# Performance work log

Measured on AMD Instinct MI355X. Metric: run time of the kernel, lower is better.

Reference implementation:

```python
import jax, jax.numpy as jnp
import numpy as np

THRESH = 0.4


def setup_inputs() -> dict:
    key = jax.random.key(0)
    ks = jax.random.split(key, 8)
    B, N, C, H, O = 8, 16384, 640, 256, 128
    s = 0.02  # small init so sigmoid(logits) ~ 0.5 -> realistic mixed selection
    return {
        "point_features": jax.random.normal(ks[0], (B, N, C), jnp.float32),
        "point_coords": jax.random.normal(ks[1], (B, N, 3), jnp.float32) * 10.0,
        "w1": jax.random.normal(ks[2], (C, H), jnp.float32) * s,
        "b1": jnp.zeros((H,), jnp.float32),
        "w2": jax.random.normal(ks[3], (H, 1), jnp.float32) * s,
        "b2": jnp.zeros((1,), jnp.float32),
        "wo": jax.random.normal(ks[4], (C, O), jnp.float32) * s,
        "bo": jnp.zeros((O,), jnp.float32),
    }


def reference(point_features, point_coords, w1, b1, w2, b2, wo, bo):
    B, N, _ = point_features.shape
    # 2-layer MLP -> per-point logit -> sigmoid score
    h = jax.nn.relu(jnp.einsum('bnc,ch->bnh', point_features, w1) + b1)
    logits = jnp.einsum('bnh,ho->bno', h, w2) + b2          # [B, N, 1]
    scores = jax.nn.sigmoid(logits)                          # [B, N, 1]
    # score-scaled features through output projection
    feats = jnp.einsum('bnc,co->bno', point_features * scores, wo) + bo  # [B, N, O]
    # score-threshold selection + per-batch stream compaction into a
    # zero-padded tensor (padded to N, the jit-static worst case)
    sel = scores[..., 0] > THRESH                            # [B, N] bool
    pos = jnp.cumsum(sel.astype(jnp.int32), axis=1) - 1      # destination slot
    pos = jnp.where(sel, pos, N)                             # unselected -> OOB (dropped)
    bidx = jnp.arange(B)[:, None]
    selected_keypoints = jnp.zeros_like(feats).at[bidx, pos].set(feats, mode='drop')
    selected_coords = jnp.zeros_like(point_coords).at[bidx, pos].set(point_coords, mode='drop')
    # point_mask: True where the row is zero padding (matches (coords==0).sum(-1)!=0)
    point_mask = jnp.sum(selected_coords == 0, axis=-1) != 0
    return selected_keypoints, selected_coords, point_mask
```

## Files before the change

kernel.cpp:

```cpp
#include <hip/hip_runtime.h>
#include <hip/hip_bf16.h>


typedef __attribute__((ext_vector_type(8))) short short8v;
typedef __attribute__((ext_vector_type(4))) float f32x4;

#define M_TOTAL 131072
#define C_DIM 640
#define H_DIM 256
#define O_DIM 128
#define NCOMB 384
#define TM 64
#define KSTEPS 20
#define N_PTS 16384
#define TILES_PER_B 256
#define NTILES 2048
#define THRL -0.4054651081f
#define FIX_MARGIN 0.03f

#define OUT_COORD_OFF 16777216
#define OUT_MASK_OFF  17170432

#define WT_OFF     0u
#define TMASK_OFF  491520u
#define TAGG_OFF   507904u
#define TEXCL_OFF  516096u
#define COUNTS_OFF 524288u
#define G_OFF      1572864u

#define LGKMCNT0 asm volatile("s_waitcnt lgkmcnt(0)" ::: "memory")
#define SBAR __builtin_amdgcn_s_barrier()

__device__ __forceinline__ unsigned int f2bf_bits(float f) {
  unsigned int u = __builtin_bit_cast(unsigned int, f);
  return (u + 0x7fffu + ((u >> 16) & 1u)) >> 16;
}
__device__ __forceinline__ unsigned int pack_bf2(float lo, float hi) {
  return f2bf_bits(lo) | (f2bf_bits(hi) << 16);
}

__global__ __launch_bounds__(256) void convert_w(const float* __restrict__ w1,
                                                 const float* __restrict__ wo,
                                                 unsigned short* __restrict__ Wt2) {
  int o = blockIdx.x * 256 + threadIdx.x;
  if (o < NCOMB * C_DIM) {
    int e = o & 7;
    int g = o >> 3;
    int pp = g & 3;
    int qq = (g >> 2) & 15;
    int tc = g >> 6;
    int ct = tc % 24;
    int t = tc / 24;
    int k = t * 32 + pp * 8 + e;
    int n = ct * 16 + qq;
    float v = (n < H_DIM) ? w1[k * H_DIM + n] : wo[k * O_DIM + (n - H_DIM)];
    Wt2[o] = (unsigned short)f2bf_bits(v);
  }
}

__global__ __launch_bounds__(512, 4) void gemm_fused(
    const float* __restrict__ pf, const unsigned short* __restrict__ Wt2,
    const float* __restrict__ w1, const float* __restrict__ b1,
    const float* __restrict__ w2, const float* __restrict__ b2,
    const float* __restrict__ bo, unsigned long long* __restrict__ tmask,
    int* __restrict__ tagg, float* __restrict__ G) {
  __shared__ __align__(16) unsigned short As[3][2048];

  const int tid = threadIdx.x;
  const int lane = tid & 63;
  const int wv = tid >> 6;
  const int q = lane & 15;
  const int p = lane >> 4;
  const int tile = blockIdx.x;
  const int m0 = tile * TM;

  f32x4 acc[3][4];
#pragma unroll
  for (int i = 0; i < 3; ++i)
#pragma unroll
    for (int rt = 0; rt < 4; ++rt) acc[i][rt] = (f32x4){0.f, 0.f, 0.f, 0.f};

  const float* asrc = pf + (size_t)(m0 + (tid >> 3)) * C_DIM + (tid & 7) * 4;
  const int aphys = ((tid >> 1) ^ ((tid >> 4) & 3)) * 8 + (tid & 1) * 4;
  const int aswz = (q >> 1) & 3;

  const unsigned short* bbase = Wt2 + wv * 512 + q * 32 + p * 8;

  float4 Rcur;
  {
    float4 R0 = *(const float4*)(asrc);
    Rcur = *(const float4*)(asrc + 32);
    *(uint2*)&As[0][aphys] = make_uint2(pack_bf2(R0.x, R0.y), pack_bf2(R0.z, R0.w));
    LGKMCNT0;
    SBAR;
  }

  int scur = 0;
#pragma unroll 1
  for (int t = 0; t < KSTEPS; ++t) {
    const unsigned short* bp = bbase + (size_t)t * 12288;
    short8v bc0 = *(const short8v*)(bp);
    short8v bc1 = *(const short8v*)(bp + 4096);
    short8v bc2 = *(const short8v*)(bp + 8192);
    int snxt = scur + 1;
    if (snxt == 3) snxt = 0;
    if (t + 2 < KSTEPS) {
      float4 Rnext = *(const float4*)(asrc + (t + 2) * 32);
      *(uint2*)&As[snxt][aphys] =
          make_uint2(pack_bf2(Rcur.x, Rcur.y), pack_bf2(Rcur.z, Rcur.w));
      Rcur = Rnext;
    } else if (t + 1 < KSTEPS) {
      *(uint2*)&As[snxt][aphys] =
          make_uint2(pack_bf2(Rcur.x, Rcur.y), pack_bf2(Rcur.z, Rcur.w));
    }
    LGKMCNT0;
    SBAR;
    short8v af[4];
#pragma unroll
    for (int rt = 0; rt < 4; ++rt)
      af[rt] = *(const short8v*)&As[scur][((rt * 64 + q * 4 + p) ^ aswz) * 8];
    __builtin_amdgcn_s_setprio(1);
#pragma unroll
    for (int rt = 0; rt < 4; ++rt) {
      acc[0][rt] = __builtin_amdgcn_mfma_f32_16x16x32_bf16(af[rt], bc0, acc[0][rt], 0, 0, 0);
      acc[1][rt] = __builtin_amdgcn_mfma_f32_16x16x32_bf16(af[rt], bc1, acc[1][rt], 0, 0, 0);
      acc[2][rt] = __builtin_amdgcn_mfma_f32_16x16x32_bf16(af[rt], bc2, acc[2][rt], 0, 0, 0);
    }
    __builtin_amdgcn_s_setprio(0);
    scur = snxt;
  }
  __syncthreads();

  float* lpart = (float*)&As[0][0];
  float* llog = (float*)&As[1][0];
  float* srow = llog + 64;
  float* fsum = srow + 64;
  unsigned long long* s_fixmask = (unsigned long long*)(fsum + 4);

  float w2v[2], b1v[2];
#pragma unroll
  for (int i = 0; i < 2; ++i) {
    int col = (wv + 8 * i) * 16 + q;
    w2v[i] = w2[col];
    b1v[i] = b1[col];
  }
#pragma unroll
  for (int rt = 0; rt < 4; ++rt) {
    float pr[4] = {0.f, 0.f, 0.f, 0.f};
#pragma unroll
    for (int i = 0; i < 2; ++i)
#pragma unroll
      for (int r = 0; r < 4; ++r)
        pr[r] += fmaxf(acc[i][rt][r] + b1v[i], 0.f) * w2v[i];
#pragma unroll
    for (int mk = 1; mk < 16; mk <<= 1)
#pragma unroll
      for (int r = 0; r < 4; ++r) pr[r] += __shfl_xor(pr[r], mk);
    if (q == 0)
#pragma unroll
      for (int r = 0; r < 4; ++r) lpart[wv * 64 + rt * 16 + p * 4 + r] = pr[r];
  }
  __syncthreads();

  bool nf = false;
  if (wv == 0) {
    float lg = b2[0];
#pragma unroll
    for (int w = 0; w < 8; ++w) lg += lpart[w * 64 + tid];
    llog[tid] = lg;
    nf = fabsf(lg - THRL) < FIX_MARGIN;
  }
  unsigned long long fm = __ballot(nf);
  if (tid == 0) *s_fixmask = fm;
  __syncthreads();

  unsigned long long fixmask = *s_fixmask;
  while (fixmask) {
    int row = __ffsll(fixmask) - 1;
    fixmask &= fixmask - 1;
    if (tid < 256) {
      const float* prow = pf + (size_t)(m0 + row) * C_DIM;
      float a0 = 0.f, a1 = 0.f;
      for (int c = 0; c < C_DIM; c += 2) {
        a0 = fmaf(prow[c], w1[(size_t)c * H_DIM + tid], a0);
        a1 = fmaf(prow[c + 1], w1[(size_t)(c + 1) * H_DIM + tid], a1);
      }
      float v = fmaxf(a0 + a1 + b1[tid], 0.f) * w2[tid];
#pragma unroll
      for (int mk = 1; mk < 64; mk <<= 1) v += __shfl_xor(v, mk);
      if (lane == 0) fsum[wv] = v;
    }
    __syncthreads();
    if (tid == 0)
      llog[row] = fsum[0] + fsum[1] + fsum[2] + fsum[3] + b2[0];
    __syncthreads();
  }

  bool sel = false;
  float flog = 0.f;
  if (wv == 0) {
    flog = llog[tid];
    sel = flog > THRL;
  }
  unsigned long long selmask = __ballot(sel);
  if (wv == 0) {
    srow[tid] = 1.f / (1.f + expf(-flog));
    if (tid == 0) {
      tmask[tile] = selmask;
      tagg[tile] = __popcll(selmask);
    }
  }
  __syncthreads();

  {
    const int gcol = wv * 16 + q;
    const float bov = bo[gcol];
#pragma unroll
    for (int rt = 0; rt < 4; ++rt)
#pragma unroll
      for (int r = 0; r < 4; ++r) {
        int row = rt * 16 + p * 4 + r;
        G[(size_t)(m0 + row) * O_DIM + gcol] = fmaf(acc[2][rt][r], srow[row], bov);
      }
  }
}

__global__ __launch_bounds__(256) void scan_tiles(const int* __restrict__ tagg,
                                                  int* __restrict__ texcl,
                                                  int* __restrict__ counts) {
  __shared__ int wsum[4];
  const int c = blockIdx.x, t = threadIdx.x;
  const int lane = t & 63, w = t >> 6;
  int v = tagg[c * 256 + t];
  int inc = v;
#pragma unroll
  for (int d = 1; d < 64; d <<= 1) {
    int n = __shfl_up(inc, d);
    if (lane >= d) inc += n;
  }
  if (lane == 63) wsum[w] = inc;
  __syncthreads();
  int base = 0;
#pragma unroll
  for (int ww = 0; ww < 4; ++ww)
    if (ww < w) base += wsum[ww];
  texcl[c * 256 + t] = base + inc - v;
  if (t == 255) counts[c] = base + inc;
}

__global__ __launch_bounds__(512) void scatter(
    const float* __restrict__ G, const unsigned long long* __restrict__ tmask,
    const int* __restrict__ texcl, const float* __restrict__ pc,
    float* __restrict__ out) {
  const int tile = blockIdx.x;
  const int tid = threadIdx.x;
  const int lane = tid & 63;
  const int wv = tid >> 6;
  const unsigned long long mask = tmask[tile];
  const int base = (tile >> 8) * N_PTS + texcl[tile];
  const int m0 = tile * TM;
#pragma unroll
  for (int j = 0; j < 8; ++j) {
    const int row = wv * 8 + j;
    if (!((mask >> row) & 1ull)) continue;
    const int dst = base + __popcll(mask & ((1ull << row) - 1ull));
    const int m = m0 + row;
    float2 g = *(const float2*)(G + (size_t)m * O_DIM + lane * 2);
    *(float2*)(out + (size_t)dst * O_DIM + lane * 2) = g;
    if (lane == 0) {
      float c0 = pc[m * 3], c1 = pc[m * 3 + 1], c2 = pc[m * 3 + 2];
      float* oc = out + OUT_COORD_OFF;
      oc[dst * 3] = c0; oc[dst * 3 + 1] = c1; oc[dst * 3 + 2] = c2;
      out[OUT_MASK_OFF + dst] = (c0 == 0.f || c1 == 0.f || c2 == 0.f) ? 1.f : 0.f;
    }
  }
}

__global__ __launch_bounds__(256) void fill_tail(const int* __restrict__ counts,
                                                 float* __restrict__ out) {
  const int lane = threadIdx.x & 63;
  for (int m = blockIdx.x * 4 + (threadIdx.x >> 6); m < M_TOTAL; m += 8192) {
    int b = m >> 14, j = m & (N_PTS - 1);
    if (j < counts[b]) continue;
    *(float2*)(out + (size_t)m * O_DIM + lane * 2) = make_float2(0.f, 0.f);
    if (lane == 0) {
      float* oc = out + OUT_COORD_OFF;
      oc[m * 3] = 0.f; oc[m * 3 + 1] = 0.f; oc[m * 3 + 2] = 0.f;
      out[OUT_MASK_OFF + m] = 1.f;
    }
  }
}

extern "C" void kernel_launch(void* const* d_in, const int* in_sizes, int n_in,
                              void* d_out, int out_size, void* d_ws, size_t ws_size,
                              hipStream_t stream) {
  const float* pf = (const float*)d_in[0];
  const float* pc = (const float*)d_in[1];
  const float* w1 = (const float*)d_in[2];
  const float* b1 = (const float*)d_in[3];
  const float* w2 = (const float*)d_in[4];
  const float* b2 = (const float*)d_in[5];
  const float* wo = (const float*)d_in[6];
  const float* bo = (const float*)d_in[7];
  float* out = (float*)d_out;
  char* ws = (char*)d_ws;

  unsigned short* Wt2 = (unsigned short*)(ws + WT_OFF);
  unsigned long long* tmask = (unsigned long long*)(ws + TMASK_OFF);
  int* tagg = (int*)(ws + TAGG_OFF);
  int* texcl = (int*)(ws + TEXCL_OFF);
  int* counts = (int*)(ws + COUNTS_OFF);
  float* G = (float*)(ws + G_OFF);

  convert_w<<<960, 256, 0, stream>>>(w1, wo, Wt2);
  gemm_fused<<<NTILES, 512, 0, stream>>>(pf, Wt2, w1, b1, w2, b2, bo,
                                         tmask, tagg, G);
  scan_tiles<<<8, 256, 0, stream>>>(tagg, texcl, counts);
  scatter<<<NTILES, 512, 0, stream>>>(G, tmask, texcl, pc, out);
  fill_tail<<<2048, 256, 0, stream>>>(counts, out);
}
```

Measured before the change: 197.5 us.

## Replicate bf16 weights, rotate K-step start per tile, prefetch B fragments

The converted weight buffer is written four times, and each tile reads the copy chosen by tile&3. Each tile also starts its K loop at a tile-dependent offset. Together these spread concurrent weight reads across different addresses and channels instead of every block hitting the same lines. The B fragments for the next K step are now loaded one iteration ahead, which hides global load latency behind the MFMAs at the cost of extra registers and a larger workspace. The summation order changes per tile, so results can differ slightly in floating point.

```diff
diff --git a/kernel.cpp b/kernel.cpp
--- a/kernel.cpp
+++ b/kernel.cpp
@@ -15,6 +15,7 @@
 #define N_PTS 16384
 #define TILES_PER_B 256
 #define NTILES 2048
+#define WT_ELEMS 245760
 #define THRL -0.4054651081f
 #define FIX_MARGIN 0.03f
 
@@ -22,11 +23,11 @@
 #define OUT_MASK_OFF  17170432
 
 #define WT_OFF     0u
-#define TMASK_OFF  491520u
-#define TAGG_OFF   507904u
-#define TEXCL_OFF  516096u
-#define COUNTS_OFF 524288u
-#define G_OFF      1572864u
+#define TMASK_OFF  1966080u
+#define TAGG_OFF   1982464u
+#define TEXCL_OFF  1990656u
+#define COUNTS_OFF 1998848u
+#define G_OFF      2621440u
 
 #define LGKMCNT0 asm volatile("s_waitcnt lgkmcnt(0)" ::: "memory")
 #define SBAR __builtin_amdgcn_s_barrier()
@@ -43,7 +44,7 @@
                                                  const float* __restrict__ wo,
                                                  unsigned short* __restrict__ Wt2) {
   int o = blockIdx.x * 256 + threadIdx.x;
-  if (o < NCOMB * C_DIM) {
+  if (o < WT_ELEMS) {
     int e = o & 7;
     int g = o >> 3;
     int pp = g & 3;
@@ -54,7 +55,9 @@
     int k = t * 32 + pp * 8 + e;
     int n = ct * 16 + qq;
     float v = (n < H_DIM) ? w1[k * H_DIM + n] : wo[k * O_DIM + (n - H_DIM)];
-    Wt2[o] = (unsigned short)f2bf_bits(v);
+    unsigned short bv = (unsigned short)f2bf_bits(v);
+#pragma unroll
+    for (int r = 0; r < 4; ++r) Wt2[(size_t)r * WT_ELEMS + o] = bv;
   }
 }
 
@@ -73,6 +76,7 @@
   const int p = lane >> 4;
   const int tile = blockIdx.x;
   const int m0 = tile * TM;
+  const int rot = tile % KSTEPS;
 
   f32x4 acc[3][4];
 #pragma unroll
@@ -84,12 +88,20 @@
   const int aphys = ((tid >> 1) ^ ((tid >> 4) & 3)) * 8 + (tid & 1) * 4;
   const int aswz = (q >> 1) & 3;
 
-  const unsigned short* bbase = Wt2 + wv * 512 + q * 32 + p * 8;
+  const unsigned short* bbase =
+      Wt2 + (size_t)(tile & 3) * WT_ELEMS + wv * 512 + q * 32 + p * 8;
 
   float4 Rcur;
+  short8v bc0, bc1, bc2;
   {
-    float4 R0 = *(const float4*)(asrc);
-    Rcur = *(const float4*)(asrc + 32);
+    float4 R0 = *(const float4*)(asrc + rot * 32);
+    const unsigned short* bp = bbase + (size_t)rot * 12288;
+    bc0 = *(const short8v*)(bp);
+    bc1 = *(const short8v*)(bp + 4096);
+    bc2 = *(const short8v*)(bp + 8192);
+    int t1 = rot + 1;
+    if (t1 >= KSTEPS) t1 -= KSTEPS;
+    Rcur = *(const float4*)(asrc + t1 * 32);
     *(uint2*)&As[0][aphys] = make_uint2(pack_bf2(R0.x, R0.y), pack_bf2(R0.z, R0.w));
     LGKMCNT0;
     SBAR;
@@ -97,19 +109,27 @@
 
   int scur = 0;
 #pragma unroll 1
-  for (int t = 0; t < KSTEPS; ++t) {
-    const unsigned short* bp = bbase + (size_t)t * 12288;
-    short8v bc0 = *(const short8v*)(bp);
-    short8v bc1 = *(const short8v*)(bp + 4096);
-    short8v bc2 = *(const short8v*)(bp + 8192);
+  for (int tt = 0; tt < KSTEPS; ++tt) {
+    short8v bn0, bn1, bn2;
+    if (tt + 1 < KSTEPS) {
+      int tn = tt + 1 + rot;
+      if (tn >= KSTEPS) tn -= KSTEPS;
+      const unsigned short* bp = bbase + (size_t)tn * 12288;
+      bn0 = *(const short8v*)(bp);
+      bn1 = *(const short8v*)(bp + 4096);
+      bn2 = *(const short8v*)(bp + 8192);
+    }
     int snxt = scur + 1;
     if (snxt == 3) snxt = 0;
-    if (t + 2 < KSTEPS) {
-      float4 Rnext = *(const float4*)(asrc + (t + 2) * 32);
+    if (tt + 2 < KSTEPS) {
+      int tnn = tt + 2 + rot;
+      if (tnn >= KSTEPS) tnn -= KSTEPS;
+      if (tnn >= KSTEPS) tnn -= KSTEPS;
+      float4 Rnext = *(const float4*)(asrc + tnn * 32);
       *(uint2*)&As[snxt][aphys] =
           make_uint2(pack_bf2(Rcur.x, Rcur.y), pack_bf2(Rcur.z, Rcur.w));
       Rcur = Rnext;
-    } else if (t + 1 < KSTEPS) {
+    } else if (tt + 1 < KSTEPS) {
       *(uint2*)&As[snxt][aphys] =
           make_uint2(pack_bf2(Rcur.x, Rcur.y), pack_bf2(Rcur.z, Rcur.w));
     }
@@ -127,6 +147,7 @@
       acc[2][rt] = __builtin_amdgcn_mfma_f32_16x16x32_bf16(af[rt], bc2, acc[2][rt], 0, 0, 0);
     }
     __builtin_amdgcn_s_setprio(0);
+    if (tt + 1 < KSTEPS) { bc0 = bn0; bc1 = bn1; bc2 = bn2; }
     scur = snxt;
   }
   __syncthreads();
```

Result: slower. 202.2 us (+2.4%).

## Enlarge GEMM M-tile to 256 rows with 4x2 wave grid for B reuse

Applied to the files above, without the earlier changes.

The fused GEMM now processes 256 rows per block instead of 64. Waves are arranged as 4 row groups by 2 column groups, each holding 12 accumulator tiles, so every B fragment loaded from global memory feeds four times as many MFMAs. The per-tile selection masks are still produced at 64-row granularity, so scan and scatter are unchanged. The cost is a much larger register footprint (48 f32x4 accumulators, with the launch-bounds occupancy hint dropped), 48KB of LDS, and only 512 blocks, which lowers occupancy and latency hiding.

```diff
diff --git a/kernel.cpp b/kernel.cpp
--- a/kernel.cpp
+++ b/kernel.cpp
@@ -10,11 +10,11 @@
 #define H_DIM 256
 #define O_DIM 128
 #define NCOMB 384
-#define TM 64
+#define TM 256
 #define KSTEPS 20
 #define N_PTS 16384
-#define TILES_PER_B 256
-#define NTILES 2048
+#define NBLOCKS 512
+#define NCHUNKS 2048
 #define THRL -0.4054651081f
 #define FIX_MARGIN 0.03f
 
@@ -37,6 +37,10 @@
 }
 __device__ __forceinline__ unsigned int pack_bf2(float lo, float hi) {
   return f2bf_bits(lo) | (f2bf_bits(hi) << 16);
+}
+
+__device__ __forceinline__ int agran(int row, int kg) {
+  return ((row << 2) + kg) ^ ((row >> 1) & 3);
 }
 
 __global__ __launch_bounds__(256) void convert_w(const float* __restrict__ w1,
@@ -58,39 +62,62 @@
   }
 }
 
-__global__ __launch_bounds__(512, 4) void gemm_fused(
+__global__ __launch_bounds__(512) void gemm_fused(
     const float* __restrict__ pf, const unsigned short* __restrict__ Wt2,
     const float* __restrict__ w1, const float* __restrict__ b1,
     const float* __restrict__ w2, const float* __restrict__ b2,
     const float* __restrict__ bo, unsigned long long* __restrict__ tmask,
     int* __restrict__ tagg, float* __restrict__ G) {
-  __shared__ __align__(16) unsigned short As[3][2048];
+  __shared__ __align__(16) unsigned short As[3][8192];
 
   const int tid = threadIdx.x;
   const int lane = tid & 63;
   const int wv = tid >> 6;
   const int q = lane & 15;
   const int p = lane >> 4;
+  const int mg = wv & 3;
+  const int ng = wv >> 2;
   const int tile = blockIdx.x;
   const int m0 = tile * TM;
 
-  f32x4 acc[3][4];
-#pragma unroll
-  for (int i = 0; i < 3; ++i)
+  f32x4 acc[12][4];
+#pragma unroll
+  for (int i = 0; i < 12; ++i)
 #pragma unroll
     for (int rt = 0; rt < 4; ++rt) acc[i][rt] = (f32x4){0.f, 0.f, 0.f, 0.f};
 
-  const float* asrc = pf + (size_t)(m0 + (tid >> 3)) * C_DIM + (tid & 7) * 4;
-  const int aphys = ((tid >> 1) ^ ((tid >> 4) & 3)) * 8 + (tid & 1) * 4;
+  const float* asrc0 = pf + (size_t)(m0 + (tid >> 3)) * C_DIM + (tid & 7) * 4;
+  const float* asrc1 = pf + (size_t)(m0 + ((tid + 512) >> 3)) * C_DIM + (tid & 7) * 4;
+  const float* asrc2 = pf + (size_t)(m0 + ((tid + 1024) >> 3)) * C_DIM + (tid & 7) * 4;
+  const float* asrc3 = pf + (size_t)(m0 + ((tid + 1536) >> 3)) * C_DIM + (tid & 7) * 4;
+  const int kh = tid & 7;
+  const int aw0 = agran((tid) >> 3, kh >> 1) * 8 + (kh & 1) * 4;
+  const int aw1 = agran((tid + 512) >> 3, kh >> 1) * 8 + (kh & 1) * 4;
+  const int aw2 = agran((tid + 1024) >> 3, kh >> 1) * 8 + (kh & 1) * 4;
+  const int aw3 = agran((tid + 1536) >> 3, kh >> 1) * 8 + (kh & 1) * 4;
   const int aswz = (q >> 1) & 3;
 
-  const unsigned short* bbase = Wt2 + wv * 512 + q * 32 + p * 8;
-
-  float4 Rcur;
+  const unsigned short* bbase = Wt2 + (size_t)(ng * 12) * 512 + (q * 4 + p) * 8;
+
+#define STAGE_CVT(slot, R0, R1, R2, R3)                                        \
+  {                                                                            \
+    *(uint2*)&As[slot][aw0] = make_uint2(pack_bf2(R0.x, R0.y), pack_bf2(R0.z, R0.w)); \
+    *(uint2*)&As[slot][aw1] = make_uint2(pack_bf2(R1.x, R1.y), pack_bf2(R1.z, R1.w)); \
+    *(uint2*)&As[slot][aw2] = make_uint2(pack_bf2(R2.x, R2.y), pack_bf2(R2.z, R2.w)); \
+    *(uint2*)&As[slot][aw3] = make_uint2(pack_bf2(R3.x, R3.y), pack_bf2(R3.z, R3.w)); \
+  }
+
+  float4 Rg0, Rg1, Rg2, Rg3;
   {
-    float4 R0 = *(const float4*)(asrc);
-    Rcur = *(const float4*)(asrc + 32);
-    *(uint2*)&As[0][aphys] = make_uint2(pack_bf2(R0.x, R0.y), pack_bf2(R0.z, R0.w));
+    float4 a0 = *(const float4*)(asrc0);
+    float4 a1 = *(const float4*)(asrc1);
+    float4 a2 = *(const float4*)(asrc2);
+    float4 a3 = *(const float4*)(asrc3);
+    STAGE_CVT(0, a0, a1, a2, a3);
+    Rg0 = *(const float4*)(asrc0 + 32);
+    Rg1 = *(const float4*)(asrc1 + 32);
+    Rg2 = *(const float4*)(asrc2 + 32);
+    Rg3 = *(const float4*)(asrc3 + 32);
     LGKMCNT0;
     SBAR;
   }
@@ -98,130 +125,148 @@
   int scur = 0;
 #pragma unroll 1
   for (int t = 0; t < KSTEPS; ++t) {
-    const unsigned short* bp = bbase + (size_t)t * 12288;
-    short8v bc0 = *(const short8v*)(bp);
-    short8v bc1 = *(const short8v*)(bp + 4096);
-    short8v bc2 = *(const short8v*)(bp + 8192);
     int snxt = scur + 1;
     if (snxt == 3) snxt = 0;
-    if (t + 2 < KSTEPS) {
-      float4 Rnext = *(const float4*)(asrc + (t + 2) * 32);
-      *(uint2*)&As[snxt][aphys] =
-          make_uint2(pack_bf2(Rcur.x, Rcur.y), pack_bf2(Rcur.z, Rcur.w));
-      Rcur = Rnext;
-    } else if (t + 1 < KSTEPS) {
-      *(uint2*)&As[snxt][aphys] =
-          make_uint2(pack_bf2(Rcur.x, Rcur.y), pack_bf2(Rcur.z, Rcur.w));
+    if (t + 1 < KSTEPS) {
+      STAGE_CVT(snxt, Rg0, Rg1, Rg2, Rg3);
+      if (t + 2 < KSTEPS) {
+        Rg0 = *(const float4*)(asrc0 + (t + 2) * 32);
+        Rg1 = *(const float4*)(asrc1 + (t + 2) * 32);
+        Rg2 = *(const float4*)(asrc2 + (t + 2) * 32);
+        Rg3 = *(const float4*)(asrc3 + (t + 2) * 32);
+      }
     }
     LGKMCNT0;
     SBAR;
     short8v af[4];
 #pragma unroll
-    for (int rt = 0; rt < 4; ++rt)
-      af[rt] = *(const short8v*)&As[scur][((rt * 64 + q * 4 + p) ^ aswz) * 8];
-    __builtin_amdgcn_s_setprio(1);
-#pragma unroll
     for (int rt = 0; rt < 4; ++rt) {
-      acc[0][rt] = __builtin_amdgcn_mfma_f32_16x16x32_bf16(af[rt], bc0, acc[0][rt], 0, 0, 0);
-      acc[1][rt] = __builtin_amdgcn_mfma_f32_16x16x32_bf16(af[rt], bc1, acc[1][rt], 0, 0, 0);
-      acc[2][rt] = __builtin_amdgcn_mfma_f32_16x16x32_bf16(af[rt], bc2, acc[2][rt], 0, 0, 0);
-    }
-    __builtin_amdgcn_s_setprio(0);
+      int row = mg * 64 + rt * 16 + q;
+      af[rt] = *(const short8v*)&As[scur][((((row << 2) + p) ^ aswz)) * 8];
+    }
+    const unsigned short* bt = bbase + (size_t)t * 12288;
+    short8v bA0, bA1, bA2, bB0, bB1, bB2;
+    bA0 = *(const short8v*)(bt);
+    bA1 = *(const short8v*)(bt + 512);
+    bA2 = *(const short8v*)(bt + 1024);
+#define MFMA3(J0, B0, B1, B2)                                                  \
+  {                                                                            \
+    _Pragma("unroll") for (int rt = 0; rt < 4; ++rt) {                         \
+      acc[J0][rt] = __builtin_amdgcn_mfma_f32_16x16x32_bf16(af[rt], B0, acc[J0][rt], 0, 0, 0);       \
+      acc[J0 + 1][rt] = __builtin_amdgcn_mfma_f32_16x16x32_bf16(af[rt], B1, acc[J0 + 1][rt], 0, 0, 0); \
+      acc[J0 + 2][rt] = __builtin_amdgcn_mfma_f32_16x16x32_bf16(af[rt], B2, acc[J0 + 2][rt], 0, 0, 0); \
+    }                                                                          \
+  }
+    bB0 = *(const short8v*)(bt + 1536);
+    bB1 = *(const short8v*)(bt + 2048);
+    bB2 = *(const short8v*)(bt + 2560);
+    MFMA3(0, bA0, bA1, bA2);
+    bA0 = *(const short8v*)(bt + 3072);
+    bA1 = *(const short8v*)(bt + 3584);
+    bA2 = *(const short8v*)(bt + 4096);
+    MFMA3(3, bB0, bB1, bB2);
+    bB0 = *(const short8v*)(bt + 4608);
+    bB1 = *(const short8v*)(bt + 5120);
+    bB2 = *(const short8v*)(bt + 5632);
+    MFMA3(6, bA0, bA1, bA2);
+    MFMA3(9, bB0, bB1, bB2);
+#undef MFMA3
     scur = snxt;
   }
   __syncthreads();
 
   float* lpart = (float*)&As[0][0];
   float* llog = (float*)&As[1][0];
-  float* srow = llog + 64;
-  float* fsum = srow + 64;
-  unsigned long long* s_fixmask = (unsigned long long*)(fsum + 4);
-
-  float w2v[2], b1v[2];
-#pragma unroll
-  for (int i = 0; i < 2; ++i) {
-    int col = (wv + 8 * i) * 16 + q;
-    w2v[i] = w2[col];
-    b1v[i] = b1[col];
-  }
-#pragma unroll
-  for (int rt = 0; rt < 4; ++rt) {
-    float pr[4] = {0.f, 0.f, 0.f, 0.f};
-#pragma unroll
-    for (int i = 0; i < 2; ++i)
-#pragma unroll
-      for (int r = 0; r < 4; ++r)
-        pr[r] += fmaxf(acc[i][rt][r] + b1v[i], 0.f) * w2v[i];
-#pragma unroll
-    for (int mk = 1; mk < 16; mk <<= 1)
-#pragma unroll
-      for (int r = 0; r < 4; ++r) pr[r] += __shfl_xor(pr[r], mk);
-    if (q == 0)
-#pragma unroll
-      for (int r = 0; r < 4; ++r) lpart[wv * 64 + rt * 16 + p * 4 + r] = pr[r];
-  }
-  __syncthreads();
-
-  bool nf = false;
-  if (wv == 0) {
-    float lg = b2[0];
-#pragma unroll
-    for (int w = 0; w < 8; ++w) lg += lpart[w * 64 + tid];
+  float* srow = llog + 256;
+  float* fsum = srow + 256;
+  unsigned long long* s_fm = (unsigned long long*)(fsum + 4);
+
+  {
+    const int nw1 = (ng == 0) ? 12 : 4;
+#pragma unroll
+    for (int rt = 0; rt < 4; ++rt) {
+      float pr[4] = {0.f, 0.f, 0.f, 0.f};
+      for (int i = 0; i < 12; ++i) {
+        if (i < nw1) {
+          int col = (ng * 12 + i) * 16 + q;
+          float b1v = b1[col], w2v = w2[col];
+#pragma unroll
+          for (int r = 0; r < 4; ++r)
+            pr[r] += fmaxf(acc[i][rt][r] + b1v, 0.f) * w2v;
+        }
+      }
+#pragma unroll
+      for (int mk = 1; mk < 16; mk <<= 1)
+#pragma unroll
+        for (int r = 0; r < 4; ++r) pr[r] += __shfl_xor(pr[r], mk);
+      if (q == 0)
+#pragma unroll
+        for (int r = 0; r < 4; ++r)
+          lpart[ng * 256 + mg * 64 + rt * 16 + p * 4 + r] = pr[r];
+    }
+  }
+  __syncthreads();
+
+  if (tid < 256) {
+    float lg = lpart[tid] + lpart[256 + tid] + b2[0];
     llog[tid] = lg;
-    nf = fabsf(lg - THRL) < FIX_MARGIN;
-  }
-  unsigned long long fm = __ballot(nf);
-  if (tid == 0) *s_fixmask = fm;
-  __syncthreads();
-
-  unsigned long long fixmask = *s_fixmask;
-  while (fixmask) {
-    int row = __ffsll(fixmask) - 1;
-    fixmask &= fixmask - 1;
-    if (tid < 256) {
-      const float* prow = pf + (size_t)(m0 + row) * C_DIM;
-      float a0 = 0.f, a1 = 0.f;
-      for (int c = 0; c < C_DIM; c += 2) {
-        a0 = fmaf(prow[c], w1[(size_t)c * H_DIM + tid], a0);
-        a1 = fmaf(prow[c + 1], w1[(size_t)(c + 1) * H_DIM + tid], a1);
+    bool nf = fabsf(lg - THRL) < FIX_MARGIN;
+    unsigned long long fm = __ballot(nf);
+    if (lane == 0) s_fm[tid >> 6] = fm;
+  }
+  __syncthreads();
+
+#pragma unroll 1
+  for (int h = 0; h < 4; ++h) {
+    unsigned long long fixmask = s_fm[h];
+    while (fixmask) {
+      int row = h * 64 + (__ffsll(fixmask) - 1);
+      fixmask &= fixmask - 1;
+      if (tid < 256) {
+        const float* prow = pf + (size_t)(m0 + row) * C_DIM;
+        float a0 = 0.f, a1 = 0.f;
+        for (int c = 0; c < C_DIM; c += 2) {
+          a0 = fmaf(prow[c], w1[(size_t)c * H_DIM + tid], a0);
+          a1 = fmaf(prow[c + 1], w1[(size_t)(c + 1) * H_DIM + tid], a1);
+        }
+        float v = fmaxf(a0 + a1 + b1[tid], 0.f) * w2[tid];
+#pragma unroll
+        for (int mk = 1; mk < 64; mk <<= 1) v += __shfl_xor(v, mk);
+        if (lane == 0) fsum[tid >> 6] = v;
       }
-      float v = fmaxf(a0 + a1 + b1[tid], 0.f) * w2[tid];
-#pragma unroll
-      for (int mk = 1; mk < 64; mk <<= 1) v += __shfl_xor(v, mk);
-      if (lane == 0) fsum[wv] = v;
-    }
-    __syncthreads();
-    if (tid == 0)
-      llog[row] = fsum[0] + fsum[1] + fsum[2] + fsum[3] + b2[0];
-    __syncthreads();
-  }
-
-  bool sel = false;
-  float flog = 0.f;
-  if (wv == 0) {
-    flog = llog[tid];
-    sel = flog > THRL;
-  }
-  unsigned long long selmask = __ballot(sel);
-  if (wv == 0) {
+      __syncthreads();
+      if (tid == 0)
+        llog[row] = fsum[0] + fsum[1] + fsum[2] + fsum[3] + b2[0];
+      __syncthreads();
+    }
+  }
+
+  if (tid < 256) {
+    float flog = llog[tid];
+    bool sel = flog > THRL;
+    unsigned long long mk = __ballot(sel);
     srow[tid] = 1.f / (1.f + expf(-flog));
-    if (tid == 0) {
-      tmask[tile] = selmask;
-      tagg[tile] = __popcll(selmask);
-    }
-  }
-  __syncthreads();
-
-  {
-    const int gcol = wv * 16 + q;
-    const float bov = bo[gcol];
-#pragma unroll
-    for (int rt = 0; rt < 4; ++rt)
-#pragma unroll
-      for (int r = 0; r < 4; ++r) {
-        int row = rt * 16 + p * 4 + r;
-        G[(size_t)(m0 + row) * O_DIM + gcol] = fmaf(acc[2][rt][r], srow[row], bov);
-      }
+    if (lane == 0) {
+      int ch = tile * 4 + (tid >> 6);
+      tmask[ch] = mk;
+      tagg[ch] = __popcll(mk);
+    }
+  }
+  __syncthreads();
+
+  if (ng == 1) {
+#pragma unroll
+    for (int i = 4; i < 12; ++i) {
+      int gcol = (i - 4) * 16 + q;
+      float bov = bo[gcol];
+#pragma unroll
+      for (int rt = 0; rt < 4; ++rt)
+#pragma unroll
+        for (int r = 0; r < 4; ++r) {
+          int row = mg * 64 + rt * 16 + p * 4 + r;
+          G[(size_t)(m0 + row) * O_DIM + gcol] = fmaf(acc[i][rt][r], srow[row], bov);
+        }
+    }
   }
 }
 
@@ -252,13 +297,13 @@
     const float* __restrict__ G, const unsigned long long* __restrict__ tmask,
     const int* __restrict__ texcl, const float* __restrict__ pc,
     float* __restrict__ out) {
-  const int tile = blockIdx.x;
+  const int ch = blockIdx.x;
   const int tid = threadIdx.x;
   const int lane = tid & 63;
   const int wv = tid >> 6;
-  const unsigned long long mask = tmask[tile];
-  const int base = (tile >> 8) * N_PTS + texcl[tile];
-  const int m0 = tile * TM;
+  const unsigned long long mask = tmask[ch];
+  const int base = (ch >> 8) * N_PTS + texcl[ch];
+  const int m0 = ch * 64;
 #pragma unroll
   for (int j = 0; j < 8; ++j) {
     const int row = wv * 8 + j;
@@ -313,9 +358,9 @@
   float* G = (float*)(ws + G_OFF);
 
   convert_w<<<960, 256, 0, stream>>>(w1, wo, Wt2);
-  gemm_fused<<<NTILES, 512, 0, stream>>>(pf, Wt2, w1, b1, w2, b2, bo,
-                                         tmask, tagg, G);
+  gemm_fused<<<NBLOCKS, 512, 0, stream>>>(pf, Wt2, w1, b1, w2, b2, bo,
+                                          tmask, tagg, G);
   scan_tiles<<<8, 256, 0, stream>>>(tagg, texcl, counts);
-  scatter<<<NTILES, 512, 0, stream>>>(G, tmask, texcl, pc, out);
+  scatter<<<NCHUNKS, 512, 0, stream>>>(G, tmask, texcl, pc, out);
   fill_tail<<<2048, 256, 0, stream>>>(counts, out);
 }
```

After: 254.1 us. 1.29x slower.

## Prefetch B fragments four k-steps ahead with 4-slot LDS ring

Applied to the files above, without the earlier changes.

Restructures the GEMM main loop into a manually unrolled four-step body that keeps B-weight fragments for four future k-steps in registers, issuing each global load four iterations before use. The A staging buffer grows from three to four LDS slots so slot indices are compile-time constants, and the priority hints are dropped. Launch bounds drop from 4 to 3 waves-per-SIMD occupancy target to make room for the extra 36 VGPRs of prefetched B. The aim is to hide global load latency for the weights, at the cost of lower occupancy and more LDS.

```diff
diff --git a/kernel.cpp b/kernel.cpp
--- a/kernel.cpp
+++ b/kernel.cpp
@@ -13,7 +13,6 @@
 #define TM 64
 #define KSTEPS 20
 #define N_PTS 16384
-#define TILES_PER_B 256
 #define NTILES 2048
 #define THRL -0.4054651081f
 #define FIX_MARGIN 0.03f
@@ -58,13 +57,13 @@
   }
 }
 
-__global__ __launch_bounds__(512, 4) void gemm_fused(
+__global__ __launch_bounds__(512, 3) void gemm_fused(
     const float* __restrict__ pf, const unsigned short* __restrict__ Wt2,
     const float* __restrict__ w1, const float* __restrict__ b1,
     const float* __restrict__ w2, const float* __restrict__ b2,
     const float* __restrict__ bo, unsigned long long* __restrict__ tmask,
     int* __restrict__ tagg, float* __restrict__ G) {
-  __shared__ __align__(16) unsigned short As[3][2048];
+  __shared__ __align__(16) unsigned short As[4][2048];
 
   const int tid = threadIdx.x;
   const int lane = tid & 63;
@@ -86,49 +85,71 @@
 
   const unsigned short* bbase = Wt2 + wv * 512 + q * 32 + p * 8;
 
+  short8v b0A, b0B, b0C, b1A, b1B, b1C, b2A, b2B, b2C, b3A, b3B, b3C;
+
+#define BLOAD(S0, S1, S2, T)                                   \
+  {                                                            \
+    const unsigned short* bp = bbase + (size_t)(T) * 12288;    \
+    S0 = *(const short8v*)(bp);                                \
+    S1 = *(const short8v*)(bp + 4096);                         \
+    S2 = *(const short8v*)(bp + 8192);                         \
+  }
+
   float4 Rcur;
   {
     float4 R0 = *(const float4*)(asrc);
+    BLOAD(b0A, b0B, b0C, 0)
+    BLOAD(b1A, b1B, b1C, 1)
+    BLOAD(b2A, b2B, b2C, 2)
+    BLOAD(b3A, b3B, b3C, 3)
     Rcur = *(const float4*)(asrc + 32);
     *(uint2*)&As[0][aphys] = make_uint2(pack_bf2(R0.x, R0.y), pack_bf2(R0.z, R0.w));
     LGKMCNT0;
     SBAR;
   }
 
-  int scur = 0;
+#define KSTEP(T, SLOT, SA, SB, SC)                                             \
+  {                                                                            \
+    if ((T) + 2 < KSTEPS) {                                                    \
+      float4 Rn = *(const float4*)(asrc + ((T) + 2) * 32);                     \
+      *(uint2*)&As[((SLOT) + 1) & 3][aphys] =                                  \
+          make_uint2(pack_bf2(Rcur.x, Rcur.y), pack_bf2(Rcur.z, Rcur.w));      \
+      Rcur = make_float4(Rn.x, Rn.y, Rn.z, Rn.w);                              \
+    } else if ((T) + 1 < KSTEPS) {                                             \
+      *(uint2*)&As[((SLOT) + 1) & 3][aphys] =                                  \
+          make_uint2(pack_bf2(Rcur.x, Rcur.y), pack_bf2(Rcur.z, Rcur.w));      \
+    }                                                                          \
+    LGKMCNT0;                                                                  \
+    SBAR;                                                                      \
+    short8v af0 = *(const short8v*)&As[SLOT][((0 * 64 + q * 4 + p) ^ aswz) * 8]; \
+    short8v af1 = *(const short8v*)&As[SLOT][((1 * 64 + q * 4 + p) ^ aswz) * 8]; \
+    short8v af2 = *(const short8v*)&As[SLOT][((2 * 64 + q * 4 + p) ^ aswz) * 8]; \
+    short8v af3 = *(const short8v*)&As[SLOT][((3 * 64 + q * 4 + p) ^ aswz) * 8]; \
+    acc[0][0] = __builtin_amdgcn_mfma_f32_16x16x32_bf16(af0, SA, acc[0][0], 0, 0, 0); \
+    acc[1][0] = __builtin_amdgcn_mfma_f32_16x16x32_bf16(af0, SB, acc[1][0], 0, 0, 0); \
+    acc[2][0] = __builtin_amdgcn_mfma_f32_16x16x32_bf16(af0, SC, acc[2][0], 0, 0, 0); \
+    acc[0][1] = __builtin_amdgcn_mfma_f32_16x16x32_bf16(af1, SA, acc[0][1], 0, 0, 0); \
+    acc[1][1] = __builtin_amdgcn_mfma_f32_16x16x32_bf16(af1, SB, acc[1][1], 0, 0, 0); \
+    acc[2][1] = __builtin_amdgcn_mfma_f32_16x16x32_bf16(af1, SC, acc[2][1], 0, 0, 0); \
+    acc[0][2] = __builtin_amdgcn_mfma_f32_16x16x32_bf16(af2, SA, acc[0][2], 0, 0, 0); \
+    acc[1][2] = __builtin_amdgcn_mfma_f32_16x16x32_bf16(af2, SB, acc[1][2], 0, 0, 0); \
+    acc[2][2] = __builtin_amdgcn_mfma_f32_16x16x32_bf16(af2, SC, acc[2][2], 0, 0, 0); \
+    acc[0][3] = __builtin_amdgcn_mfma_f32_16x16x32_bf16(af3, SA, acc[0][3], 0, 0, 0); \
+    acc[1][3] = __builtin_amdgcn_mfma_f32_16x16x32_bf16(af3, SB, acc[1][3], 0, 0, 0); \
+    acc[2][3] = __builtin_amdgcn_mfma_f32_16x16x32_bf16(af3, SC, acc[2][3], 0, 0, 0); \
+    if ((T) + 4 < KSTEPS) BLOAD(SA, SB, SC, (T) + 4)                           \
+  }
+
 #pragma unroll 1
-  for (int t = 0; t < KSTEPS; ++t) {
-    const unsigned short* bp = bbase + (size_t)t * 12288;
-    short8v bc0 = *(const short8v*)(bp);
-    short8v bc1 = *(const short8v*)(bp + 4096);
-    short8v bc2 = *(const short8v*)(bp + 8192);
-    int snxt = scur + 1;
-    if (snxt == 3) snxt = 0;
-    if (t + 2 < KSTEPS) {
-      float4 Rnext = *(const float4*)(asrc + (t + 2) * 32);
-      *(uint2*)&As[snxt][aphys] =
-          make_uint2(pack_bf2(Rcur.x, Rcur.y), pack_bf2(Rcur.z, Rcur.w));
-      Rcur = Rnext;
-    } else if (t + 1 < KSTEPS) {
-      *(uint2*)&As[snxt][aphys] =
-          make_uint2(pack_bf2(Rcur.x, Rcur.y), pack_bf2(Rcur.z, Rcur.w));
-    }
-    LGKMCNT0;
-    SBAR;
-    short8v af[4];
-#pragma unroll
-    for (int rt = 0; rt < 4; ++rt)
-      af[rt] = *(const short8v*)&As[scur][((rt * 64 + q * 4 + p) ^ aswz) * 8];
-    __builtin_amdgcn_s_setprio(1);
-#pragma unroll
-    for (int rt = 0; rt < 4; ++rt) {
-      acc[0][rt] = __builtin_amdgcn_mfma_f32_16x16x32_bf16(af[rt], bc0, acc[0][rt], 0, 0, 0);
-      acc[1][rt] = __builtin_amdgcn_mfma_f32_16x16x32_bf16(af[rt], bc1, acc[1][rt], 0, 0, 0);
-      acc[2][rt] = __builtin_amdgcn_mfma_f32_16x16x32_bf16(af[rt], bc2, acc[2][rt], 0, 0, 0);
-    }
-    __builtin_amdgcn_s_setprio(0);
-    scur = snxt;
-  }
+  for (int i = 0; i < 5; ++i) {
+    const int t0 = i * 4;
+    KSTEP(t0 + 0, 0, b0A, b0B, b0C)
+    KSTEP(t0 + 1, 1, b1A, b1B, b1C)
+    KSTEP(t0 + 2, 2, b2A, b2B, b2C)
+    KSTEP(t0 + 3, 3, b3A, b3B, b3C)
+  }
+#undef KSTEP
+#undef BLOAD
   __syncthreads();
 
   float* lpart = (float*)&As[0][0];
```

Measured after the change: 254.0 us. 28.6% more time.
